# Kernel optimization log

Measured on AMD Instinct MI355X. Metric: run time of the kernel, lower is better.

Reference implementation:

```python
import jax, jax.numpy as jnp
import numpy as np

SIMS = 16
AMP = 1.0  # cfg['attention_amplifier']


def setup_inputs() -> dict:
    key = jax.random.key(0)
    k1, k2, k3 = jax.random.split(key, 3)
    B, F = 32, 2048
    data = jax.random.normal(k1, (B * SIMS, F), dtype=jnp.float32)
    attention = jax.random.normal(k2, (B * SIMS, F), dtype=jnp.float32)
    W = jax.random.normal(k3, (SIMS, 2 * SIMS), dtype=jnp.float32) * (1.0 / np.sqrt(2 * SIMS))
    b = jnp.zeros((SIMS,), dtype=jnp.float32)
    return {"data": data, "attention": attention, "W": W, "b": b}


def reference(data, attention, W, b):
    s = SIMS
    B = data.shape[0] // s
    inputs = data.reshape(B, s, -1)            # [B, s, F]
    attn_in = attention.reshape(B, s, -1)      # [B, s, G]
    # bmm(inputs^T, attention) -> [B, F, G]
    a = jnp.einsum('bsf,bsg->bfg', inputs, attn_in)
    a = jax.nn.log_softmax(a, axis=1)          # log_softmax over F dim (dim=1)
    # bmm(a, attention^T) -> [B, F, s]
    a = jnp.einsum('bfg,bsg->bfs', a, attn_in)
    concat = jnp.concatenate([jnp.swapaxes(a, 1, 2), inputs], axis=1)  # [B, 2s, F]
    concat = jnp.swapaxes(concat, 1, 2).reshape(-1, 2 * s)             # [B*F, 2s]
    gate = jax.nn.sigmoid(concat @ W.T + b)    # [B*F, s]
    # output.t().contiguous().view(data.shape): [s, B*F] row-major -> [B*s, F]
    gate = gate.T.reshape(data.shape)
    return gate * data * AMP
```

## Files before the change

kernel.cpp:

```cpp
#include <hip/hip_runtime.h>
#include <math.h>

#define LOG2E 1.44269504088896340736f
#define LN2   0.69314718055994530942f

typedef _Float16 half8 __attribute__((ext_vector_type(8)));
typedef float f32x4v __attribute__((ext_vector_type(4)));

#define AROW 24

template <bool ATOMIC>
__global__ __launch_bounds__(256, 4) void kA(const float* __restrict__ data,
                                             const float* __restrict__ attn,
                                             float* __restrict__ Lout) {
    __shared__ _Float16 AhB[128 * AROW];
    __shared__ _Float16 AlB[128 * AROW];
    const int tid = threadIdx.x;
    const int lin = blockIdx.x;
    const int b = lin & 31, fb = (lin >> 5) & 3, gb = lin >> 7;
    const int wave = tid >> 6, lane = tid & 63;
    const int n = lane & 15, q = lane >> 4;
    const int s0 = (q & 1) * 8;

    const float* Tb = attn + (size_t)b * 16 * 2048;
    half8 B1[2], B2[2];
#pragma unroll
    for (int ct = 0; ct < 2; ++ct) {
        const int g = gb * 128 + wave * 32 + ct * 16 + n;
        half8 bh, bl;
#pragma unroll
        for (int j = 0; j < 8; ++j) {
            float x = Tb[(size_t)(s0 + j) * 2048 + g] * LOG2E;
            _Float16 h = (_Float16)x;
            _Float16 l = (_Float16)(x - (float)h);
            bh[j] = h;
            bl[j] = (q < 2) ? l : (_Float16)0.0f;
        }
        B1[ct] = bh;
        B2[ct] = bl;
    }

    f32x4v cs0 = {0.f, 0.f, 0.f, 0.f}, cs1 = {0.f, 0.f, 0.f, 0.f};

    const float* Ab = data + (size_t)b * 16 * 2048 + fb * 512;
    const int fst = tid & 127;
    const int sh  = (tid >> 7) * 8;
    const _Float16* aptr = ((q < 2) ? AhB : AlB) + n * AROW + s0;

    for (int chunk = 0; chunk < 4; ++chunk) {
        const float* Ac = Ab + chunk * 128;
        _Float16 hb[8], lb[8];
#pragma unroll
        for (int j = 0; j < 8; ++j) {
            float x = Ac[(size_t)(sh + j) * 2048 + fst];
            _Float16 h = (_Float16)x;
            hb[j] = h;
            lb[j] = (_Float16)(x - (float)h);
        }
        __syncthreads();
        half8 hv, lv;
#pragma unroll
        for (int j = 0; j < 8; ++j) { hv[j] = hb[j]; lv[j] = lb[j]; }
        *(half8*)(AhB + fst * AROW + sh) = hv;
        *(half8*)(AlB + fst * AROW + sh) = lv;
        __syncthreads();

#pragma unroll
        for (int rt = 0; rt < 8; ++rt) {
            half8 af = *(const half8*)(aptr + rt * 16 * AROW);
            f32x4v C = {0.f, 0.f, 0.f, 0.f};
            C = __builtin_amdgcn_mfma_f32_16x16x32_f16(af, B1[0], C, 0, 0, 0);
            C = __builtin_amdgcn_mfma_f32_16x16x32_f16(af, B2[0], C, 0, 0, 0);
            cs0[0] += __builtin_amdgcn_exp2f(C[0]);
            cs0[1] += __builtin_amdgcn_exp2f(C[1]);
            cs0[2] += __builtin_amdgcn_exp2f(C[2]);
            cs0[3] += __builtin_amdgcn_exp2f(C[3]);
            f32x4v D = {0.f, 0.f, 0.f, 0.f};
            D = __builtin_amdgcn_mfma_f32_16x16x32_f16(af, B1[1], D, 0, 0, 0);
            D = __builtin_amdgcn_mfma_f32_16x16x32_f16(af, B2[1], D, 0, 0, 0);
            cs1[0] += __builtin_amdgcn_exp2f(D[0]);
            cs1[1] += __builtin_amdgcn_exp2f(D[1]);
            cs1[2] += __builtin_amdgcn_exp2f(D[2]);
            cs1[3] += __builtin_amdgcn_exp2f(D[3]);
        }
    }

    float v0 = cs0[0] + cs0[1] + cs0[2] + cs0[3];
    float v1 = cs1[0] + cs1[1] + cs1[2] + cs1[3];
    v0 += __shfl_xor(v0, 16);
    v0 += __shfl_xor(v0, 32);
    v1 += __shfl_xor(v1, 16);
    v1 += __shfl_xor(v1, 32);
    if (q == 0) {
        const int g = gb * 128 + wave * 32 + n;
        if (ATOMIC) {
            atomicAdd(&Lout[(size_t)b * 2048 + g], v0);
            atomicAdd(&Lout[(size_t)b * 2048 + g + 16], v1);
        } else {
            Lout[((size_t)fb * 32 + b) * 2048 + g] = v0;
            Lout[((size_t)fb * 32 + b) * 2048 + g + 16] = v1;
        }
    }
}

#define TP 260
__global__ __launch_bounds__(256) void kTail(const float* __restrict__ attn,
                                             const float* __restrict__ Lpart, int nparts,
                                             float* __restrict__ Mpart,
                                             float* __restrict__ cpart) {
    __shared__ float Tsh[16 * TP];
    __shared__ float Lsh[256];
    __shared__ float red[16][17];
    const int tid = threadIdx.x;
    const int seg = blockIdx.x, b = blockIdx.y;
    const int g0 = seg * 256;

#pragma unroll
    for (int s = 0; s < 16; ++s)
        Tsh[s * TP + tid] = attn[(size_t)(b * 16 + s) * 2048 + g0 + tid];
    {
        float sum = 0.f;
        for (int p = 0; p < nparts; ++p)
            sum += Lpart[((size_t)p * 32 + b) * 2048 + g0 + tid];
        Lsh[tid] = LN2 * __builtin_amdgcn_logf(sum);
    }
    __syncthreads();

    {
        const int t = tid & 15, i = tid >> 4;
        float acc = 0.f;
#pragma unroll
        for (int k = 0; k < 4; ++k) {
            float4 l  = *(const float4*)(Lsh + i * 16 + k * 4);
            float4 tv = *(const float4*)(Tsh + t * TP + i * 16 + k * 4);
            acc += l.x * tv.x + l.y * tv.y + l.z * tv.z + l.w * tv.w;
        }
        red[t][i] = acc;
    }
    __syncthreads();
    if (tid < 16) {
        float s = 0.f;
#pragma unroll
        for (int k = 0; k < 16; ++k) s += red[tid][k];
        cpart[((size_t)seg * 32 + b) * 16 + tid] = s;
    }

    {
        const int s = tid >> 4, t = tid & 15;
        float a0 = 0.f, a1 = 0.f;
#pragma unroll 4
        for (int qk = 0; qk < 32; ++qk) {
            float4 x = *(const float4*)(Tsh + s * TP + qk * 8);
            float4 y = *(const float4*)(Tsh + t * TP + qk * 8);
            a0 += x.x * y.x + x.y * y.y + x.z * y.z + x.w * y.w;
            float4 x2 = *(const float4*)(Tsh + s * TP + qk * 8 + 4);
            float4 y2 = *(const float4*)(Tsh + t * TP + qk * 8 + 4);
            a1 += x2.x * y2.x + x2.y * y2.y + x2.z * y2.z + x2.w * y2.w;
        }
        Mpart[((size_t)seg * 32 + b) * 256 + tid] = a0 + a1;
    }
}

__global__ __launch_bounds__(256) void kC2(const float* __restrict__ data,
                                           const float* __restrict__ Mpart,
                                           const float* __restrict__ cpart,
                                           const float* __restrict__ W,
                                           const float* __restrict__ bias,
                                           float* __restrict__ out) {
    __shared__ float Msh[256];
    __shared__ float csh[16];
    __shared__ float Vsh[256];
    __shared__ float w0sh[16];
    const int tid = threadIdx.x;
    const int b = blockIdx.y;
    const int f = blockIdx.x * 256 + tid;

    {
        float m = 0.f;
#pragma unroll
        for (int p = 0; p < 8; ++p) m += Mpart[((size_t)p * 32 + b) * 256 + tid];
        Msh[tid] = m;
        if (tid < 16) {
            float c = 0.f;
#pragma unroll
            for (int p = 0; p < 8; ++p) c += cpart[((size_t)p * 32 + b) * 16 + tid];
            csh[tid] = c;
        }
    }
    __syncthreads();
    {
        const int s = tid >> 4, j = tid & 15;
        float acc = 0.f;
#pragma unroll
        for (int t = 0; t < 16; ++t) acc += Msh[s * 16 + t] * W[j * 32 + t];
        Vsh[s * 16 + j] = acc + W[j * 32 + 16 + s];
        if (s == 0) {
            float w0 = 0.f;
#pragma unroll
            for (int t = 0; t < 16; ++t) w0 += csh[t] * W[j * 32 + t];
            w0sh[j] = bias[j] - w0;
        }
    }
    __syncthreads();

    float As[16];
#pragma unroll
    for (int s = 0; s < 16; ++s)
        As[s] = data[(size_t)(b * 16 + s) * 2048 + f];
#pragma unroll
    for (int j = 0; j < 16; ++j) {
        float p = w0sh[j];
#pragma unroll
        for (int s = 0; s < 16; ++s) p += As[s] * Vsh[s * 16 + j];
        float e = __builtin_amdgcn_exp2f(-LOG2E * p);
        float gate = __builtin_amdgcn_rcpf(1.0f + e);
        size_t r = (size_t)(j * 32 + b) * 2048 + f;
        out[r] = gate * data[r];
    }
}

extern "C" void kernel_launch(void* const* d_in, const int* in_sizes, int n_in,
                              void* d_out, int out_size, void* d_ws, size_t ws_size,
                              hipStream_t stream) {
    const float* data = (const float*)d_in[0];
    const float* attn = (const float*)d_in[1];
    const float* W    = (const float*)d_in[2];
    const float* bias = (const float*)d_in[3];
    float* out = (float*)d_out;
    float* ws  = (float*)d_ws;

    const size_t LP = 4 * 32 * 2048;
    const size_t need_big = LP + 65536 + 4096;

    if (ws_size >= need_big * sizeof(float)) {
        float* Lpart = ws;
        float* Mpart = ws + LP;
        float* cpart = Mpart + 65536;
        kA<false><<<dim3(2048, 1, 1), 256, 0, stream>>>(data, attn, Lpart);
        kTail<<<dim3(8, 32), 256, 0, stream>>>(attn, Lpart, 4, Mpart, cpart);
        kC2<<<dim3(8, 32), 256, 0, stream>>>(data, Mpart, cpart, W, bias, out);
    } else {
        float* Lsum  = ws;
        float* Mpart = ws + 65536;
        float* cpart = Mpart + 65536;
        hipMemsetAsync(Lsum, 0, 65536 * sizeof(float), stream);
        kA<true><<<dim3(2048, 1, 1), 256, 0, stream>>>(data, attn, Lsum);
        kTail<<<dim3(8, 32), 256, 0, stream>>>(attn, Lsum, 1, Mpart, cpart);
        kC2<<<dim3(8, 32), 256, 0, stream>>>(data, Mpart, cpart, W, bias, out);
    }
}
```

Before: 94.46 us.

## Prefetch next data chunk in kA and double block counts for tail kernels

In kA, the global loads for the next 128-column chunk are now issued into registers after the shared-memory store barrier, so they overlap the MFMA and exp work of the current chunk. The kTail and kC2 kernels are repartitioned to 128-wide segments with 16 segments per batch, doubling the grid to 512 blocks for better GPU occupancy. kC2 now splits the 16 gate outputs across two half-blocks. This raises register pressure in kA, and the reductions in kC2 now read twice as many partials.

```diff
diff --git a/kernel.cpp b/kernel.cpp
--- a/kernel.cpp
+++ b/kernel.cpp
@@ -47,23 +47,29 @@
     const int sh  = (tid >> 7) * 8;
     const _Float16* aptr = ((q < 2) ? AhB : AlB) + n * AROW + s0;
 
+    float x[8];
+#pragma unroll
+    for (int j = 0; j < 8; ++j) x[j] = Ab[(size_t)(sh + j) * 2048 + fst];
+
     for (int chunk = 0; chunk < 4; ++chunk) {
-        const float* Ac = Ab + chunk * 128;
-        _Float16 hb[8], lb[8];
+        half8 hv, lv;
 #pragma unroll
         for (int j = 0; j < 8; ++j) {
-            float x = Ac[(size_t)(sh + j) * 2048 + fst];
-            _Float16 h = (_Float16)x;
-            hb[j] = h;
-            lb[j] = (_Float16)(x - (float)h);
+            float v = x[j];
+            _Float16 h = (_Float16)v;
+            hv[j] = h;
+            lv[j] = (_Float16)(v - (float)h);
         }
         __syncthreads();
-        half8 hv, lv;
-#pragma unroll
-        for (int j = 0; j < 8; ++j) { hv[j] = hb[j]; lv[j] = lb[j]; }
         *(half8*)(AhB + fst * AROW + sh) = hv;
         *(half8*)(AlB + fst * AROW + sh) = lv;
         __syncthreads();
+
+        if (chunk < 3) {
+            const float* Ac = Ab + (chunk + 1) * 128;
+#pragma unroll
+            for (int j = 0; j < 8; ++j) x[j] = Ac[(size_t)(sh + j) * 2048 + fst];
+        }
 
 #pragma unroll
         for (int rt = 0; rt < 8; ++rt) {
@@ -103,22 +109,27 @@
     }
 }
 
-#define TP 260
+#define TP2 132
 __global__ __launch_bounds__(256) void kTail(const float* __restrict__ attn,
                                              const float* __restrict__ Lpart, int nparts,
                                              float* __restrict__ Mpart,
                                              float* __restrict__ cpart) {
-    __shared__ float Tsh[16 * TP];
-    __shared__ float Lsh[256];
+    __shared__ float Tsh[16 * TP2];
+    __shared__ float Lsh[128];
     __shared__ float red[16][17];
     const int tid = threadIdx.x;
     const int seg = blockIdx.x, b = blockIdx.y;
-    const int g0 = seg * 256;
-
-#pragma unroll
-    for (int s = 0; s < 16; ++s)
-        Tsh[s * TP + tid] = attn[(size_t)(b * 16 + s) * 2048 + g0 + tid];
-    {
+    const int g0 = seg * 128;
+
+    {
+        const int gcol = tid & 127, sh = (tid >> 7) * 8;
+#pragma unroll
+        for (int j = 0; j < 8; ++j) {
+            const int s = sh + j;
+            Tsh[s * TP2 + gcol] = attn[(size_t)(b * 16 + s) * 2048 + g0 + gcol];
+        }
+    }
+    if (tid < 128) {
         float sum = 0.f;
         for (int p = 0; p < nparts; ++p)
             sum += Lpart[((size_t)p * 32 + b) * 2048 + g0 + tid];
@@ -130,9 +141,9 @@
         const int t = tid & 15, i = tid >> 4;
         float acc = 0.f;
 #pragma unroll
-        for (int k = 0; k < 4; ++k) {
-            float4 l  = *(const float4*)(Lsh + i * 16 + k * 4);
-            float4 tv = *(const float4*)(Tsh + t * TP + i * 16 + k * 4);
+        for (int k = 0; k < 2; ++k) {
+            float4 l  = *(const float4*)(Lsh + i * 8 + k * 4);
+            float4 tv = *(const float4*)(Tsh + t * TP2 + i * 8 + k * 4);
             acc += l.x * tv.x + l.y * tv.y + l.z * tv.z + l.w * tv.w;
         }
         red[t][i] = acc;
@@ -149,18 +160,19 @@
         const int s = tid >> 4, t = tid & 15;
         float a0 = 0.f, a1 = 0.f;
 #pragma unroll 4
-        for (int qk = 0; qk < 32; ++qk) {
-            float4 x = *(const float4*)(Tsh + s * TP + qk * 8);
-            float4 y = *(const float4*)(Tsh + t * TP + qk * 8);
+        for (int qk = 0; qk < 16; ++qk) {
+            float4 x = *(const float4*)(Tsh + s * TP2 + qk * 8);
+            float4 y = *(const float4*)(Tsh + t * TP2 + qk * 8);
             a0 += x.x * y.x + x.y * y.y + x.z * y.z + x.w * y.w;
-            float4 x2 = *(const float4*)(Tsh + s * TP + qk * 8 + 4);
-            float4 y2 = *(const float4*)(Tsh + t * TP + qk * 8 + 4);
+            float4 x2 = *(const float4*)(Tsh + s * TP2 + qk * 8 + 4);
+            float4 y2 = *(const float4*)(Tsh + t * TP2 + qk * 8 + 4);
             a1 += x2.x * y2.x + x2.y * y2.y + x2.z * y2.z + x2.w * y2.w;
         }
         Mpart[((size_t)seg * 32 + b) * 256 + tid] = a0 + a1;
     }
 }
 
+#define NSEG 16
 __global__ __launch_bounds__(256) void kC2(const float* __restrict__ data,
                                            const float* __restrict__ Mpart,
                                            const float* __restrict__ cpart,
@@ -173,17 +185,18 @@
     __shared__ float w0sh[16];
     const int tid = threadIdx.x;
     const int b = blockIdx.y;
-    const int f = blockIdx.x * 256 + tid;
+    const int f = blockIdx.x * 128 + (tid & 127);
+    const int jh = tid >> 7;
 
     {
         float m = 0.f;
 #pragma unroll
-        for (int p = 0; p < 8; ++p) m += Mpart[((size_t)p * 32 + b) * 256 + tid];
+        for (int p = 0; p < NSEG; ++p) m += Mpart[((size_t)p * 32 + b) * 256 + tid];
         Msh[tid] = m;
         if (tid < 16) {
             float c = 0.f;
 #pragma unroll
-            for (int p = 0; p < 8; ++p) c += cpart[((size_t)p * 32 + b) * 16 + tid];
+            for (int p = 0; p < NSEG; ++p) c += cpart[((size_t)p * 32 + b) * 16 + tid];
             csh[tid] = c;
         }
     }
@@ -208,7 +221,8 @@
     for (int s = 0; s < 16; ++s)
         As[s] = data[(size_t)(b * 16 + s) * 2048 + f];
 #pragma unroll
-    for (int j = 0; j < 16; ++j) {
+    for (int jj = 0; jj < 8; ++jj) {
+        const int j = jh * 8 + jj;
         float p = w0sh[j];
 #pragma unroll
         for (int s = 0; s < 16; ++s) p += As[s] * Vsh[s * 16 + j];
@@ -230,22 +244,24 @@
     float* ws  = (float*)d_ws;
 
     const size_t LP = 4 * 32 * 2048;
-    const size_t need_big = LP + 65536 + 4096;
+    const size_t MP = NSEG * 32 * 256;
+    const size_t CP = NSEG * 32 * 16;
+    const size_t need_big = LP + MP + CP;
 
     if (ws_size >= need_big * sizeof(float)) {
         float* Lpart = ws;
         float* Mpart = ws + LP;
-        float* cpart = Mpart + 65536;
+        float* cpart = Mpart + MP;
         kA<false><<<dim3(2048, 1, 1), 256, 0, stream>>>(data, attn, Lpart);
-        kTail<<<dim3(8, 32), 256, 0, stream>>>(attn, Lpart, 4, Mpart, cpart);
-        kC2<<<dim3(8, 32), 256, 0, stream>>>(data, Mpart, cpart, W, bias, out);
+        kTail<<<dim3(16, 32), 256, 0, stream>>>(attn, Lpart, 4, Mpart, cpart);
+        kC2<<<dim3(16, 32), 256, 0, stream>>>(data, Mpart, cpart, W, bias, out);
     } else {
         float* Lsum  = ws;
         float* Mpart = ws + 65536;
-        float* cpart = Mpart + 65536;
+        float* cpart = Mpart + MP;
         hipMemsetAsync(Lsum, 0, 65536 * sizeof(float), stream);
         kA<true><<<dim3(2048, 1, 1), 256, 0, stream>>>(data, attn, Lsum);
-        kTail<<<dim3(8, 32), 256, 0, stream>>>(attn, Lsum, 1, Mpart, cpart);
-        kC2<<<dim3(8, 32), 256, 0, stream>>>(data, Mpart, cpart, W, bias, out);
-    }
-}
+        kTail<<<dim3(16, 32), 256, 0, stream>>>(attn, Lsum, 1, Mpart, cpart);
+        kC2<<<dim3(16, 32), 256, 0, stream>>>(data, Mpart, cpart, W, bias, out);
+    }
+}
```

Result: no change. 94.09 us (-0.4%).
